# Kernel optimization log

Hardware: AMD Instinct MI355X
Metric: run time of the kernel (lower is better)

Reference implementation:

```python
import jax, jax.numpy as jnp
import numpy as np
from jax import lax

EPS = 1e-08


def setup_inputs() -> dict:
    key = jax.random.key(0)
    k1, k2, k3 = jax.random.split(key, 3)
    B, I, O, H, W_, K = 16, 512, 512, 32, 32, 3
    x = jax.random.normal(k1, (B, I, H, W_), dtype=jnp.float32)
    s = jax.random.uniform(k2, (B, I), dtype=jnp.float32)
    weight = jax.random.normal(k3, (O, I, K, K), dtype=jnp.float32)
    return {"x": x, "s": s, "weight": weight}


def reference(x, s, weight):
    # x: [B, I, H, W], s: [B, I], weight: [O, I, kH, kW]
    B, I, H, Wd = x.shape
    O = weight.shape[0]
    # Per-sample modulated weights: [B, O, I, kH, kW]
    # (faithful to source: the weight_scale multiply is dead code, overwritten)
    Wm = s[:, None, :, None, None] * weight[None]
    # Demodulation: L2-normalize each per-sample output filter
    sigma = jnp.sqrt(jnp.sum(Wm * Wm, axis=(2, 3, 4), keepdims=True) + EPS)
    Wm = Wm / sigma
    # Grouped conv with groups = batch_size (same trick as torch source)
    x_g = x.reshape(1, B * I, H, Wd)
    W_g = Wm.reshape(B * O, I, *weight.shape[-2:])
    out = lax.conv_general_dilated(
        x_g, W_g,
        window_strides=(1, 1),
        padding='SAME',
        feature_group_count=B,
        dimension_numbers=('NCHW', 'OIHW', 'NCHW'),
    )
    return out.reshape(B, O, out.shape[-2], out.shape[-1])
```

## Files before the change

kernel.cpp:

```cpp
#include <hip/hip_runtime.h>
#include <hip/hip_bf16.h>
#include <stdint.h>

#define BATCH 16
#define CIN   512
#define COUT  512
#define HH    32
#define WW    32
#define HP    34
#define HWN   1024
#define EPS_  1e-8f

typedef __attribute__((ext_vector_type(8))) short bf16x8;
typedef __attribute__((ext_vector_type(4))) float f32x4;
typedef __attribute__((address_space(1))) void gvoid;
typedef __attribute__((address_space(3))) void lvoid;

#define XS_OFF    0
#define XS_BYTES  (BATCH*HP*HP*CIN*2)
#define WT_OFF    (XS_OFF + XS_BYTES)
#define WT_BYTES  (9*COUT*CIN*2)
#define WSQ_OFF   (WT_OFF + WT_BYTES)
#define WSQ_BYTES (COUT*CIN*4)
#define ISG_OFF   (WSQ_OFF + WSQ_BYTES)

__global__ void prep_weight(const float* __restrict__ w,
                            __hip_bfloat16* __restrict__ wt,
                            float* __restrict__ wsq) {
  int idx = blockIdx.x * 256 + threadIdx.x;
  if (idx >= COUT * CIN) return;
  const float* wp = w + (size_t)idx * 9;
  float ss = 0.f;
#pragma unroll
  for (int k = 0; k < 9; ++k) {
    float v = wp[k];
    ss += v * v;
    wt[(size_t)k * COUT * CIN + idx] = __float2bfloat16(v);
  }
  wsq[idx] = ss;
}

__global__ void calc_isig(const float* __restrict__ s,
                          const float* __restrict__ wsq,
                          float* __restrict__ isg) {
  int b = blockIdx.x >> 9;
  int o = blockIdx.x & 511;
  int l = threadIdx.x;
  const float* sp = s + b * CIN;
  const float* wq = wsq + o * CIN;
  float acc = 0.f;
  for (int i = l; i < CIN; i += 64) {
    float sv = sp[i];
    acc += sv * sv * wq[i];
  }
#pragma unroll
  for (int off = 32; off; off >>= 1) acc += __shfl_xor(acc, off);
  if (l == 0) isg[blockIdx.x] = 1.0f / sqrtf(acc + EPS_);
}

__global__ void zero_borders(__hip_bfloat16* __restrict__ xs) {
  int e = blockIdx.x % 132;
  int b = blockIdx.x / 132;
  int l = threadIdx.x;
  int hp, wp;
  if (e < 34)      { hp = 0;  wp = e; }
  else if (e < 68) { hp = 33; wp = e - 34; }
  else { int f = e - 68; hp = 1 + (f >> 1); wp = (f & 1) ? 33 : 0; }
  int4* dst = (int4*)(xs + (((size_t)(b * HP + hp)) * HP + wp) * CIN);
  dst[l] = make_int4(0, 0, 0, 0);
}

__global__ __launch_bounds__(256)
void pack_x2(const float* __restrict__ x,
             const float* __restrict__ s,
             __hip_bfloat16* __restrict__ xs) {
  __shared__ unsigned short tile[32][520];
  __shared__ float ssh[CIN];
  const int bid = blockIdx.x;
  const int h = bid & 31;
  const int b = bid >> 5;
  const int tid = threadIdx.x;

  ssh[tid]       = s[b * CIN + tid];
  ssh[256 + tid] = s[b * CIN + 256 + tid];
  __syncthreads();

  const int r = tid >> 3;
  const int c = tid & 7;
  const float* xbase = x + (size_t)b * CIN * HWN + h * WW;
#pragma unroll
  for (int p = 0; p < 16; ++p) {
    int i = p * 32 + r;
    float4 v = *(const float4*)(xbase + (size_t)i * HWN + c * 4);
    float sc = ssh[i];
#pragma unroll
    for (int j = 0; j < 4; ++j) {
      float f = ((const float*)&v)[j] * sc;
      __hip_bfloat16 hb = __float2bfloat16(f);
      tile[c * 4 + j][i] = *(unsigned short*)&hb;
    }
  }
  __syncthreads();

  const int w  = tid >> 3;
  const int i0 = (tid & 7) * 64;
  __hip_bfloat16* dst = xs + (((size_t)(b * HP + h + 1)) * HP + (w + 1)) * CIN + i0;
  const int4* src = (const int4*)&tile[w][i0];
#pragma unroll
  for (int q = 0; q < 8; ++q)
    ((int4*)dst)[q] = src[q];
}

__global__ __launch_bounds__(256, 2)
void conv_mfma(const __hip_bfloat16* __restrict__ xs,
               const __hip_bfloat16* __restrict__ wt,
               const float* __restrict__ isg,
               float* __restrict__ out) {
  __shared__ __align__(16) char lds[32768];
  char* ldsA = lds;
  char* ldsB = lds + 16384;

  const int bid = blockIdx.x;
  const int nt = bid & 7;
  const int mt = (bid >> 3) & 3;
  const int b  = bid >> 5;
  const int m0  = mt * 128;
  const int hw0 = nt * 128;

  const int t  = threadIdx.x;
  const int wv = t >> 6;
  const int l  = t & 63;
  const int wr = wv >> 1;
  const int wc = wv & 1;
  const int segbase = wv * 4;

  int baseA[4], baseB[4];
#pragma unroll
  for (int q = 0; q < 4; ++q) {
    int seg = segbase + q;
    int r = seg * 8 + (l >> 3);
    int swz = (l & 7) ^ (l >> 3);
    baseA[q] = (m0 + r) * CIN + swz * 8;
    int n_abs = hw0 + r;
    int hB = n_abs >> 5, wB = n_abs & 31;
    baseB[q] = ((b * HP + hB) * HP + wB) * CIN + swz * 8;
  }

  int offA[2][4], offB[2][4];
#pragma unroll
  for (int kk = 0; kk < 2; ++kk) {
#pragma unroll
    for (int f = 0; f < 4; ++f) {
      int slot = ((kk * 4) + (l >> 4)) ^ (l & 7);
      offA[kk][f] = (wr * 64 + f * 16 + (l & 15)) * 128 + slot * 16;
      offB[kk][f] = (wc * 64 + f * 16 + (l & 15)) * 128 + slot * 16;
    }
  }

  f32x4 acc[4][4];
#pragma unroll
  for (int m = 0; m < 4; ++m)
#pragma unroll
    for (int n = 0; n < 4; ++n)
      acc[m][n] = (f32x4){0.f, 0.f, 0.f, 0.f};

  for (int kh = 0; kh < 3; ++kh) {
    for (int kw = 0; kw < 3; ++kw) {
      const int uA0 = (kh * 3 + kw) * COUT * CIN;
      const int uB0 = (kh * HP + kw) * CIN;
      for (int ic = 0; ic < 8; ++ic) {
        const int i0 = ic * 64;
#pragma unroll
        for (int q = 0; q < 4; ++q)
          __builtin_amdgcn_global_load_lds(
              (gvoid*)(const void*)(wt + uA0 + i0 + baseA[q]),
              (lvoid*)(ldsA + (segbase + q) * 1024), 16, 0, 0);
#pragma unroll
        for (int q = 0; q < 4; ++q)
          __builtin_amdgcn_global_load_lds(
              (gvoid*)(const void*)(xs + uB0 + i0 + baseB[q]),
              (lvoid*)(ldsB + (segbase + q) * 1024), 16, 0, 0);
        __syncthreads();
#pragma unroll
        for (int kk = 0; kk < 2; ++kk) {
          bf16x8 af[4], bfr[4];
#pragma unroll
          for (int f = 0; f < 4; ++f) af[f]  = *(const bf16x8*)(ldsA + offA[kk][f]);
#pragma unroll
          for (int f = 0; f < 4; ++f) bfr[f] = *(const bf16x8*)(ldsB + offB[kk][f]);
#pragma unroll
          for (int m = 0; m < 4; ++m)
#pragma unroll
            for (int n = 0; n < 4; ++n)
              acc[m][n] = __builtin_amdgcn_mfma_f32_16x16x32_bf16(
                  af[m], bfr[n], acc[m][n], 0, 0, 0);
        }
        __syncthreads();
      }
    }
  }

#pragma unroll
  for (int m = 0; m < 4; ++m) {
#pragma unroll
    for (int j = 0; j < 4; ++j) {
      int o = m0 + wr * 64 + m * 16 + (l >> 4) * 4 + j;
      float sg = isg[b * COUT + o];
      float* orow = out + ((size_t)(b * COUT + o)) * HWN + hw0 + wc * 64 + (l & 15);
#pragma unroll
      for (int n = 0; n < 4; ++n)
        orow[n * 16] = acc[m][n][j] * sg;
    }
  }
}

extern "C" void kernel_launch(void* const* d_in, const int* in_sizes, int n_in,
                              void* d_out, int out_size, void* d_ws, size_t ws_size,
                              hipStream_t stream) {
  const float* x = (const float*)d_in[0];
  const float* s = (const float*)d_in[1];
  const float* w = (const float*)d_in[2];
  float* out = (float*)d_out;
  char* ws = (char*)d_ws;
  __hip_bfloat16* xs  = (__hip_bfloat16*)(ws + XS_OFF);
  __hip_bfloat16* wt  = (__hip_bfloat16*)(ws + WT_OFF);
  float*          wsq = (float*)(ws + WSQ_OFF);
  float*          isg = (float*)(ws + ISG_OFF);

  hipLaunchKernelGGL(prep_weight, dim3((COUT * CIN + 255) / 256), dim3(256), 0, stream,
                     w, wt, wsq);
  hipLaunchKernelGGL(zero_borders, dim3(BATCH * 132), dim3(64), 0, stream, xs);
  hipLaunchKernelGGL(pack_x2, dim3(BATCH * 32), dim3(256), 0, stream, x, s, xs);
  hipLaunchKernelGGL(calc_isig, dim3(BATCH * COUT), dim3(64), 0, stream,
                     s, wsq, isg);
  hipLaunchKernelGGL(conv_mfma, dim3(BATCH * 4 * 8), dim3(256), 0, stream,
                     xs, wt, isg, out);
}
```

Baseline: 176.2 us.

## Rewrite conv as triple-buffered 8-wave pipeline and fuse prep kernels

The main conv kernel now uses 512 threads per block and a 128x256 output tile with 256 blocks. It triple-buffers LDS across 72 K-tiles and issues global-to-LDS loads for tile t+2 interleaved with MFMA phases, adding setprio and barriers; a remapped block order is meant to improve L2 reuse. The weight prep and sigma computation are fused into one kernel, and border zeroing is folded into the pack kernel, cutting launches from five to three. The risks are 144KB of dynamic LDS limiting occupancy, extra barriers per tile, and the fragile vmcnt-based synchronisation.

```diff
diff --git a/kernel.cpp b/kernel.cpp
--- a/kernel.cpp
+++ b/kernel.cpp
@@ -11,6 +11,11 @@
 #define HWN   1024
 #define EPS_  1e-8f
 
+#define NTILES 72
+#define SLOTA  16384
+#define SLOTB  32768
+#define LDS_BYTES (3*(SLOTA+SLOTB))
+
 typedef __attribute__((ext_vector_type(8))) short bf16x8;
 typedef __attribute__((ext_vector_type(4))) float f32x4;
 typedef __attribute__((address_space(1))) void gvoid;
@@ -20,71 +25,85 @@
 #define XS_BYTES  (BATCH*HP*HP*CIN*2)
 #define WT_OFF    (XS_OFF + XS_BYTES)
 #define WT_BYTES  (9*COUT*CIN*2)
-#define WSQ_OFF   (WT_OFF + WT_BYTES)
-#define WSQ_BYTES (COUT*CIN*4)
-#define ISG_OFF   (WSQ_OFF + WSQ_BYTES)
-
-__global__ void prep_weight(const float* __restrict__ w,
-                            __hip_bfloat16* __restrict__ wt,
-                            float* __restrict__ wsq) {
-  int idx = blockIdx.x * 256 + threadIdx.x;
-  if (idx >= COUT * CIN) return;
-  const float* wp = w + (size_t)idx * 9;
-  float ss = 0.f;
-#pragma unroll
-  for (int k = 0; k < 9; ++k) {
-    float v = wp[k];
-    ss += v * v;
-    wt[(size_t)k * COUT * CIN + idx] = __float2bfloat16(v);
-  }
-  wsq[idx] = ss;
-}
-
-__global__ void calc_isig(const float* __restrict__ s,
-                          const float* __restrict__ wsq,
-                          float* __restrict__ isg) {
-  int b = blockIdx.x >> 9;
-  int o = blockIdx.x & 511;
-  int l = threadIdx.x;
-  const float* sp = s + b * CIN;
-  const float* wq = wsq + o * CIN;
-  float acc = 0.f;
-  for (int i = l; i < CIN; i += 64) {
-    float sv = sp[i];
-    acc += sv * sv * wq[i];
-  }
-#pragma unroll
-  for (int off = 32; off; off >>= 1) acc += __shfl_xor(acc, off);
-  if (l == 0) isg[blockIdx.x] = 1.0f / sqrtf(acc + EPS_);
-}
-
-__global__ void zero_borders(__hip_bfloat16* __restrict__ xs) {
-  int e = blockIdx.x % 132;
-  int b = blockIdx.x / 132;
-  int l = threadIdx.x;
-  int hp, wp;
-  if (e < 34)      { hp = 0;  wp = e; }
-  else if (e < 68) { hp = 33; wp = e - 34; }
-  else { int f = e - 68; hp = 1 + (f >> 1); wp = (f & 1) ? 33 : 0; }
-  int4* dst = (int4*)(xs + (((size_t)(b * HP + hp)) * HP + wp) * CIN);
-  dst[l] = make_int4(0, 0, 0, 0);
-}
+#define ISG_OFF   (WT_OFF + WT_BYTES)
 
 __global__ __launch_bounds__(256)
-void pack_x2(const float* __restrict__ x,
-             const float* __restrict__ s,
-             __hip_bfloat16* __restrict__ xs) {
+void wprep(const float* __restrict__ w, const float* __restrict__ s,
+           __hip_bfloat16* __restrict__ wt, float* __restrict__ isg) {
+  __shared__ float s2[BATCH * CIN];
+  __shared__ float red[16][4];
+  const int o = blockIdx.x;
+  const int t = threadIdx.x;
+
+  for (int j = t; j < BATCH * CIN; j += 256) {
+    float v = s[j];
+    s2[j] = v * v;
+  }
+
+  float ss[2];
+#pragma unroll
+  for (int u = 0; u < 2; ++u) {
+    int i = t + u * 256;
+    const float* wp = w + ((size_t)o * CIN + i) * 9;
+    float acc = 0.f;
+#pragma unroll
+    for (int k = 0; k < 9; ++k) {
+      float v = wp[k];
+      acc += v * v;
+      __hip_bfloat16 hb = __float2bfloat16(v);
+      wt[(size_t)k * COUT * CIN + o * CIN + i] = hb;
+    }
+    ss[u] = acc;
+  }
+  __syncthreads();
+
+  float accb[16];
+#pragma unroll
+  for (int b = 0; b < 16; ++b) accb[b] = 0.f;
+#pragma unroll
+  for (int u = 0; u < 2; ++u) {
+    int i = t + u * 256;
+    float q = ss[u];
+#pragma unroll
+    for (int b = 0; b < 16; ++b) accb[b] += q * s2[b * CIN + i];
+  }
+#pragma unroll
+  for (int b = 0; b < 16; ++b) {
+#pragma unroll
+    for (int off = 32; off; off >>= 1) accb[b] += __shfl_xor(accb[b], off);
+    if ((t & 63) == 0) red[b][t >> 6] = accb[b];
+  }
+  __syncthreads();
+  if (t < 16) {
+    float tot = red[t][0] + red[t][1] + red[t][2] + red[t][3];
+    isg[t * COUT + o] = 1.0f / sqrtf(tot + EPS_);
+  }
+}
+
+__global__ __launch_bounds__(256)
+void pack3(const float* __restrict__ x, const float* __restrict__ s,
+           __hip_bfloat16* __restrict__ xs) {
+  const int bid = blockIdx.x;
+  const int hp = bid % 34;
+  const int b = bid / 34;
+  const int tid = threadIdx.x;
+  __hip_bfloat16* rowbase = xs + (((size_t)(b * HP + hp)) * HP) * CIN;
+
+  if (hp == 0 || hp == 33) {
+    for (int j = tid; j < HP * CIN / 8; j += 256)
+      ((int4*)rowbase)[j] = make_int4(0, 0, 0, 0);
+    return;
+  }
+  if (tid < 64)        ((int4*)rowbase)[tid] = make_int4(0, 0, 0, 0);
+  else if (tid < 128)  ((int4*)(rowbase + 33 * CIN))[tid - 64] = make_int4(0, 0, 0, 0);
+
   __shared__ unsigned short tile[32][520];
   __shared__ float ssh[CIN];
-  const int bid = blockIdx.x;
-  const int h = bid & 31;
-  const int b = bid >> 5;
-  const int tid = threadIdx.x;
-
   ssh[tid]       = s[b * CIN + tid];
   ssh[256 + tid] = s[b * CIN + 256 + tid];
   __syncthreads();
 
+  const int h = hp - 1;
   const int r = tid >> 3;
   const int c = tid & 7;
   const float* xbase = x + (size_t)b * CIN * HWN + h * WW;
@@ -102,45 +121,48 @@
   }
   __syncthreads();
 
-  const int w  = tid >> 3;
+  const int wq = tid >> 3;
   const int i0 = (tid & 7) * 64;
-  __hip_bfloat16* dst = xs + (((size_t)(b * HP + h + 1)) * HP + (w + 1)) * CIN + i0;
-  const int4* src = (const int4*)&tile[w][i0];
+  __hip_bfloat16* dst = rowbase + (wq + 1) * CIN + i0;
+  const int4* src = (const int4*)&tile[wq][i0];
 #pragma unroll
   for (int q = 0; q < 8; ++q)
     ((int4*)dst)[q] = src[q];
 }
 
-__global__ __launch_bounds__(256, 2)
-void conv_mfma(const __hip_bfloat16* __restrict__ xs,
-               const __hip_bfloat16* __restrict__ wt,
-               const float* __restrict__ isg,
-               float* __restrict__ out) {
-  __shared__ __align__(16) char lds[32768];
+__global__ __launch_bounds__(512, 2)
+void conv_mfma8(const __hip_bfloat16* __restrict__ xs,
+                const __hip_bfloat16* __restrict__ wt,
+                const float* __restrict__ isg,
+                float* __restrict__ out) {
+  extern __shared__ __align__(16) char lds[];
   char* ldsA = lds;
-  char* ldsB = lds + 16384;
+  char* ldsB = lds + 3 * SLOTA;
 
   const int bid = blockIdx.x;
-  const int nt = bid & 7;
-  const int mt = (bid >> 3) & 3;
-  const int b  = bid >> 5;
+  const int lin = (bid & 7) * 32 + (bid >> 3);
+  const int b  = lin >> 4;
+  const int mt = (lin >> 2) & 3;
+  const int nt = lin & 3;
   const int m0  = mt * 128;
-  const int hw0 = nt * 128;
+  const int hw0 = nt * 256;
 
   const int t  = threadIdx.x;
   const int wv = t >> 6;
   const int l  = t & 63;
-  const int wr = wv >> 1;
-  const int wc = wv & 1;
-  const int segbase = wv * 4;
-
-  int baseA[4], baseB[4];
+  const int wr = wv >> 2;
+  const int wc = wv & 3;
+
+  int baseA[2], baseB[4];
+  const int swz = (l & 7) ^ (l >> 3);
+#pragma unroll
+  for (int q = 0; q < 2; ++q) {
+    int r = (wv * 2 + q) * 8 + (l >> 3);
+    baseA[q] = (m0 + r) * CIN + swz * 8;
+  }
 #pragma unroll
   for (int q = 0; q < 4; ++q) {
-    int seg = segbase + q;
-    int r = seg * 8 + (l >> 3);
-    int swz = (l & 7) ^ (l >> 3);
-    baseA[q] = (m0 + r) * CIN + swz * 8;
+    int r = (wv * 4 + q) * 8 + (l >> 3);
     int n_abs = hw0 + r;
     int hB = n_abs >> 5, wB = n_abs & 31;
     baseB[q] = ((b * HP + hB) * HP + wB) * CIN + swz * 8;
@@ -151,9 +173,9 @@
   for (int kk = 0; kk < 2; ++kk) {
 #pragma unroll
     for (int f = 0; f < 4; ++f) {
-      int slot = ((kk * 4) + (l >> 4)) ^ (l & 7);
-      offA[kk][f] = (wr * 64 + f * 16 + (l & 15)) * 128 + slot * 16;
-      offB[kk][f] = (wc * 64 + f * 16 + (l & 15)) * 128 + slot * 16;
+      int slot16 = ((kk * 4) + (l >> 4)) ^ (l & 7);
+      offA[kk][f] = (wr * 64 + f * 16 + (l & 15)) * 128 + slot16 * 16;
+      offB[kk][f] = (wc * 64 + f * 16 + (l & 15)) * 128 + slot16 * 16;
     }
   }
 
@@ -164,40 +186,79 @@
     for (int n = 0; n < 4; ++n)
       acc[m][n] = (f32x4){0.f, 0.f, 0.f, 0.f};
 
-  for (int kh = 0; kh < 3; ++kh) {
-    for (int kw = 0; kw < 3; ++kw) {
-      const int uA0 = (kh * 3 + kw) * COUT * CIN;
-      const int uB0 = (kh * HP + kw) * CIN;
-      for (int ic = 0; ic < 8; ++ic) {
-        const int i0 = ic * 64;
-#pragma unroll
-        for (int q = 0; q < 4; ++q)
-          __builtin_amdgcn_global_load_lds(
-              (gvoid*)(const void*)(wt + uA0 + i0 + baseA[q]),
-              (lvoid*)(ldsA + (segbase + q) * 1024), 16, 0, 0);
-#pragma unroll
-        for (int q = 0; q < 4; ++q)
-          __builtin_amdgcn_global_load_lds(
-              (gvoid*)(const void*)(xs + uB0 + i0 + baseB[q]),
-              (lvoid*)(ldsB + (segbase + q) * 1024), 16, 0, 0);
-        __syncthreads();
-#pragma unroll
-        for (int kk = 0; kk < 2; ++kk) {
-          bf16x8 af[4], bfr[4];
-#pragma unroll
-          for (int f = 0; f < 4; ++f) af[f]  = *(const bf16x8*)(ldsA + offA[kk][f]);
-#pragma unroll
-          for (int f = 0; f < 4; ++f) bfr[f] = *(const bf16x8*)(ldsB + offB[kk][f]);
-#pragma unroll
-          for (int m = 0; m < 4; ++m)
-#pragma unroll
-            for (int n = 0; n < 4; ++n)
-              acc[m][n] = __builtin_amdgcn_mfma_f32_16x16x32_bf16(
-                  af[m], bfr[n], acc[m][n], 0, 0, 0);
-        }
-        __syncthreads();
-      }
-    }
+#define TILE_OFFS(tt, gA, gB)                                   \
+  {                                                             \
+    int tap = (tt) >> 3, ic = (tt) & 7;                         \
+    int kh = (tap * 11) >> 5;                                   \
+    int kw = tap - kh * 3;                                      \
+    gA = tap * (COUT * CIN) + ic * 64;                          \
+    gB = (kh * HP + kw) * CIN + ic * 64;                        \
+  }
+
+#define STAGE_A(q, gA, sl)                                                  \
+  __builtin_amdgcn_global_load_lds(                                         \
+      (gvoid*)(const void*)(wt + (gA) + baseA[q]),                          \
+      (lvoid*)(ldsA + (sl) * SLOTA + (wv * 2 + (q)) * 1024), 16, 0, 0)
+#define STAGE_B(q, gB, sl)                                                  \
+  __builtin_amdgcn_global_load_lds(                                         \
+      (gvoid*)(const void*)(xs + (gB) + baseB[q]),                          \
+      (lvoid*)(ldsB + (sl) * SLOTB + (wv * 4 + (q)) * 1024), 16, 0, 0)
+
+  {
+    int gA, gB;
+    TILE_OFFS(0, gA, gB);
+    STAGE_A(0, gA, 0); STAGE_A(1, gA, 0);
+    STAGE_B(0, gB, 0); STAGE_B(1, gB, 0); STAGE_B(2, gB, 0); STAGE_B(3, gB, 0);
+    TILE_OFFS(1, gA, gB);
+    STAGE_A(0, gA, 1); STAGE_A(1, gA, 1);
+    STAGE_B(0, gB, 1); STAGE_B(1, gB, 1); STAGE_B(2, gB, 1); STAGE_B(3, gB, 1);
+  }
+  asm volatile("s_waitcnt vmcnt(6)" ::: "memory");
+  __builtin_amdgcn_s_barrier();
+
+#define PHASE(mp, kk, STAGES)                                                         \
+  {                                                                                   \
+    bf16x8 af0 = *(const bf16x8*)(pA + offA[kk][2 * (mp)]);                           \
+    bf16x8 af1 = *(const bf16x8*)(pA + offA[kk][2 * (mp) + 1]);                       \
+    if ((mp) == 0) {                                                                  \
+      bfr0 = *(const bf16x8*)(pB + offB[kk][0]);                                      \
+      bfr1 = *(const bf16x8*)(pB + offB[kk][1]);                                      \
+      bfr2 = *(const bf16x8*)(pB + offB[kk][2]);                                      \
+      bfr3 = *(const bf16x8*)(pB + offB[kk][3]);                                      \
+    }                                                                                 \
+    STAGES;                                                                           \
+    __builtin_amdgcn_s_barrier();                                                     \
+    __builtin_amdgcn_s_setprio(1);                                                    \
+    acc[2*(mp)][0]   = __builtin_amdgcn_mfma_f32_16x16x32_bf16(af0, bfr0, acc[2*(mp)][0],   0,0,0); \
+    acc[2*(mp)][1]   = __builtin_amdgcn_mfma_f32_16x16x32_bf16(af0, bfr1, acc[2*(mp)][1],   0,0,0); \
+    acc[2*(mp)][2]   = __builtin_amdgcn_mfma_f32_16x16x32_bf16(af0, bfr2, acc[2*(mp)][2],   0,0,0); \
+    acc[2*(mp)][3]   = __builtin_amdgcn_mfma_f32_16x16x32_bf16(af0, bfr3, acc[2*(mp)][3],   0,0,0); \
+    acc[2*(mp)+1][0] = __builtin_amdgcn_mfma_f32_16x16x32_bf16(af1, bfr0, acc[2*(mp)+1][0], 0,0,0); \
+    acc[2*(mp)+1][1] = __builtin_amdgcn_mfma_f32_16x16x32_bf16(af1, bfr1, acc[2*(mp)+1][1], 0,0,0); \
+    acc[2*(mp)+1][2] = __builtin_amdgcn_mfma_f32_16x16x32_bf16(af1, bfr2, acc[2*(mp)+1][2], 0,0,0); \
+    acc[2*(mp)+1][3] = __builtin_amdgcn_mfma_f32_16x16x32_bf16(af1, bfr3, acc[2*(mp)+1][3], 0,0,0); \
+    __builtin_amdgcn_s_setprio(0);                                                    \
+    __builtin_amdgcn_s_barrier();                                                     \
+  }
+
+  int cur = 0, s2 = 2;
+  bf16x8 bfr0, bfr1, bfr2, bfr3;
+  for (int tt = 0; tt < NTILES; ++tt) {
+    int t2 = tt + 2;
+    if (t2 >= NTILES) t2 = NTILES - 1;
+    int gA2, gB2;
+    TILE_OFFS(t2, gA2, gB2);
+    const char* pA = ldsA + cur * SLOTA;
+    const char* pB = ldsB + cur * SLOTB;
+
+    PHASE(0, 0, { STAGE_A(0, gA2, s2); STAGE_A(1, gA2, s2); });
+    PHASE(1, 0, { STAGE_B(0, gB2, s2); STAGE_B(1, gB2, s2); });
+    PHASE(0, 1, { STAGE_B(2, gB2, s2); });
+    PHASE(1, 1, { STAGE_B(3, gB2, s2);
+                  asm volatile("s_waitcnt vmcnt(6)" ::: "memory"); });
+
+    cur = (cur == 2) ? 0 : cur + 1;
+    s2  = (s2  == 2) ? 0 : s2  + 1;
   }
 
 #pragma unroll
@@ -224,15 +285,13 @@
   char* ws = (char*)d_ws;
   __hip_bfloat16* xs  = (__hip_bfloat16*)(ws + XS_OFF);
   __hip_bfloat16* wt  = (__hip_bfloat16*)(ws + WT_OFF);
-  float*          wsq = (float*)(ws + WSQ_OFF);
   float*          isg = (float*)(ws + ISG_OFF);
 
-  hipLaunchKernelGGL(prep_weight, dim3((COUT * CIN + 255) / 256), dim3(256), 0, stream,
-                     w, wt, wsq);
-  hipLaunchKernelGGL(zero_borders, dim3(BATCH * 132), dim3(64), 0, stream, xs);
-  hipLaunchKernelGGL(pack_x2, dim3(BATCH * 32), dim3(256), 0, stream, x, s, xs);
-  hipLaunchKernelGGL(calc_isig, dim3(BATCH * COUT), dim3(64), 0, stream,
-                     s, wsq, isg);
-  hipLaunchKernelGGL(conv_mfma, dim3(BATCH * 4 * 8), dim3(256), 0, stream,
+  (void)hipFuncSetAttribute((const void*)conv_mfma8,
+                            hipFuncAttributeMaxDynamicSharedMemorySize, LDS_BYTES);
+
+  hipLaunchKernelGGL(wprep, dim3(COUT), dim3(256), 0, stream, w, s, wt, isg);
+  hipLaunchKernelGGL(pack3, dim3(BATCH * 34), dim3(256), 0, stream, x, s, xs);
+  hipLaunchKernelGGL(conv_mfma8, dim3(256), dim3(512), LDS_BYTES, stream,
                      xs, wt, isg, out);
 }
```

After: 170.2 us. 1.04x faster.
